# Optimization experiments

Measured on AMD Instinct MI355X. Metric: run time of the kernel, lower is better.

The kernel has to match this reference:

```python
import jax, jax.numpy as jnp
import numpy as np

D_MODEL = 1024
N_HEADS = 16
D_K = D_MODEL // N_HEADS
LOCAL_WINDOW = 128
GLOBAL_TOKENS = 16


def sparse_mask(seq_len):
    i = jnp.arange(seq_len)[:, None]
    j = jnp.arange(seq_len)[None, :]
    local = jnp.abs(i - j) <= LOCAL_WINDOW
    glob = (i < GLOBAL_TOKENS) | (j < GLOBAL_TOKENS)
    causal = j <= i
    return ((local | glob) & causal)[None, None]  # [1,1,S,S]


def setup_inputs() -> dict:
    key = jax.random.key(0)
    ks = jax.random.split(key, 11)
    B, S = 2, 2048
    std = 1.0 / np.sqrt(D_MODEL)
    inp = {
        'query': jax.random.normal(ks[0], (B, S, D_MODEL), jnp.float32),
        'key': jax.random.normal(ks[1], (B, S, D_MODEL), jnp.float32),
        'value': jax.random.normal(ks[2], (B, S, D_MODEL), jnp.float32),
        'w_q': jax.random.normal(ks[3], (D_MODEL, D_MODEL), jnp.float32) * std,
        'b_q': jnp.zeros((D_MODEL,), jnp.float32),
        'w_k': jax.random.normal(ks[4], (D_MODEL, D_MODEL), jnp.float32) * std,
        'b_k': jnp.zeros((D_MODEL,), jnp.float32),
        'w_v': jax.random.normal(ks[5], (D_MODEL, D_MODEL), jnp.float32) * std,
        'b_v': jnp.zeros((D_MODEL,), jnp.float32),
        'w_o': jax.random.normal(ks[6], (D_MODEL, D_MODEL), jnp.float32) * std,
        'b_o': jnp.zeros((D_MODEL,), jnp.float32),
    }
    return inp


def reference(query, key, value, w_q, b_q, w_k, b_k, w_v, b_v, w_o, b_o):
    B, S, _ = query.shape
    # project and split heads -> [B,H,S,d_k]
    def proj(x, w, b):
        y = x @ w.T + b
        return y.reshape(B, S, N_HEADS, D_K).transpose(0, 2, 1, 3)
    q = proj(query, w_q, b_q)
    k = proj(key, w_k, b_k)
    v = proj(value, w_v, b_v)
    scores = jnp.einsum('bhqd,bhkd->bhqk', q, k) / np.sqrt(D_K).astype(np.float32)
    mask = sparse_mask(S)
    scores = jnp.where(mask, scores, -jnp.inf)
    attn = jax.nn.softmax(scores, axis=-1)
    out = jnp.einsum('bhqk,bhkd->bhqd', attn, v)
    out = out.transpose(0, 2, 1, 3).reshape(B, S, D_MODEL)
    return out @ w_o.T + b_o
```

## Files before the change

kernel.cpp:

```cpp
#include <hip/hip_runtime.h>

typedef unsigned short u16;
typedef u16 u16x8 __attribute__((ext_vector_type(8)));
typedef __bf16 bf16x8 __attribute__((ext_vector_type(8)));
typedef float f32x4 __attribute__((ext_vector_type(4)));

#define MFMA16 __builtin_amdgcn_mfma_f32_16x16x32_bf16

__device__ __forceinline__ u16 f2bf(float f) {
  unsigned u = __builtin_bit_cast(unsigned, f);
  u += 0x7FFFu + ((u >> 16) & 1u);
  return (u16)(u >> 16);
}

__device__ __forceinline__ int swz(int row, int bcol) {
  return row * 128 + (bcol ^ ((row & 7) << 4));
}

__device__ __forceinline__ void gl16(const u16* g, u16* l) {
  __builtin_amdgcn_global_load_lds(
      (const __attribute__((address_space(1))) unsigned int*)g,
      (__attribute__((address_space(3))) unsigned int*)l, 16, 0, 0);
}

__device__ __forceinline__ void BARR() {
  asm volatile("" ::: "memory");
  __builtin_amdgcn_s_barrier();
  asm volatile("" ::: "memory");
}

__global__ __launch_bounds__(256)
void cast7(const float* __restrict__ a0, const float* __restrict__ a1,
           const float* __restrict__ a2, const float* __restrict__ a3,
           const float* __restrict__ a4, const float* __restrict__ a5,
           const float* __restrict__ a6, u16* __restrict__ ws) {
  const int y = blockIdx.y;
  const float* s;
  u16* d;
  int n;
  switch (y) {
    case 0: s = a0; d = ws + 4194304; n = 4194304; break;
    case 1: s = a1; d = ws + 8388608; n = 4194304; break;
    case 2: s = a2; d = ws + 12582912; n = 4194304; break;
    case 3: s = a3; d = ws + 0; n = 1048576; break;
    case 4: s = a4; d = ws + 1048576; n = 1048576; break;
    case 5: s = a5; d = ws + 2097152; n = 1048576; break;
    default: s = a6; d = ws + 3145728; n = 1048576; break;
  }
  const int i = (blockIdx.x * 256 + threadIdx.x) * 8;
  if (i >= n) return;
  float4 v0 = *(const float4*)(s + i);
  float4 v1 = *(const float4*)(s + i + 4);
  u16x8 p = {f2bf(v0.x), f2bf(v0.y), f2bf(v0.z), f2bf(v0.w),
             f2bf(v1.x), f2bf(v1.y), f2bf(v1.z), f2bf(v1.w)};
  *(u16x8*)(d + i) = p;
}

#define STGA(tt, c)                                                         \
  gl16(A + (m0 + (c)*64 + (w << 3) + (lane >> 3)) * 1024 + (tt)*64 +        \
           (((lane & 7) ^ (lane >> 3)) << 3),                               \
       (u16*)(sb + (((tt)&1) << 16) + (c)*8192 + (w << 10)))
#define STGB(tt, c)                                                         \
  gl16(B + (n0 + (c)*64 + (w << 3) + (lane >> 3)) * 1024 + (tt)*64 +        \
           (((lane & 7) ^ (lane >> 3)) << 3),                               \
       (u16*)(sb + (((tt)&1) << 16) + 32768 + (c)*8192 + (w << 10)))

__global__ __launch_bounds__(512)
void qkv_gemm256(const u16* __restrict__ ws_in, const float* __restrict__ c0,
                 const float* __restrict__ c1, const float* __restrict__ c2,
                 u16* __restrict__ o0, u16* __restrict__ o1,
                 u16* __restrict__ o2) {
  const int bid = blockIdx.x;
  const int s = (bid & 7) * 24 + (bid >> 3);
  const int z = s >> 6;
  const int rem = s & 63;
  const int m0 = (rem >> 2) << 8;
  const int n0 = (rem & 3) << 8;

  const u16* __restrict__ A = ws_in + 4194304 + z * 4194304;
  const u16* __restrict__ B = ws_in + z * 1048576;
  const float* Bi = (z == 0) ? c0 : (z == 1) ? c1 : c2;
  u16* O = (z == 0) ? o0 : (z == 1) ? o1 : o2;

  const int tid = threadIdx.x, lane = tid & 63, w = tid >> 6;
  const int wm = w >> 2, wn = w & 3;
  const int r = lane & 15, g = lane >> 4;

  __shared__ u16 SH[65536];
  char* sb = (char*)SH;

  f32x4 acc[8][4] = {};
  bf16x8 af[2][4], bf[2][4];

  const int colr0 = (g * 16) ^ ((r & 7) << 4);
  const int colr1 = (64 + g * 16) ^ ((r & 7) << 4);
  const int rowAb = (wm * 128 + r) * 128;
  const int rowBb = 32768 + (wn * 64 + r) * 128;

#define LDA(half)                                                           \
  _Pragma("unroll") for (int m = 0; m < 4; ++m) {                           \
    char* p = sb + bo + rowAb + ((half)*64 + m * 16) * 128;                 \
    af[0][m] = __builtin_bit_cast(bf16x8, *(const u16x8*)(p + colr0));      \
    af[1][m] = __builtin_bit_cast(bf16x8, *(const u16x8*)(p + colr1));      \
  }
#define LDB(n)                                                              \
  {                                                                         \
    char* p = sb + bo + rowBb + (n)*16 * 128;                               \
    bf[0][n] = __builtin_bit_cast(bf16x8, *(const u16x8*)(p + colr0));      \
    bf[1][n] = __builtin_bit_cast(bf16x8, *(const u16x8*)(p + colr1));      \
  }
#define FMA(mh, nl)                                                         \
  __builtin_amdgcn_s_setprio(1);                                           \
  _Pragma("unroll") for (int m = 0; m < 4; ++m)                             \
  _Pragma("unroll") for (int n = 0; n < 2; ++n) {                           \
    acc[(mh)*4 + m][(nl)*2 + n] =                                           \
        MFMA16(af[0][m], bf[0][(nl)*2 + n], acc[(mh)*4 + m][(nl)*2 + n], 0, \
               0, 0);                                                       \
    acc[(mh)*4 + m][(nl)*2 + n] =                                           \
        MFMA16(af[1][m], bf[1][(nl)*2 + n], acc[(mh)*4 + m][(nl)*2 + n], 0, \
               0, 0);                                                       \
  }                                                                         \
  __builtin_amdgcn_s_setprio(0);

#pragma unroll
  for (int c = 0; c < 4; ++c) STGB(0, c);
#pragma unroll
  for (int c = 0; c < 4; ++c) STGA(0, c);
#pragma unroll
  for (int c = 0; c < 4; ++c) STGB(1, c);
#pragma unroll
  for (int c = 0; c < 4; ++c) STGA(1, c);
  asm volatile("s_waitcnt vmcnt(8)" ::: "memory");
  __builtin_amdgcn_s_barrier();
  asm volatile("" ::: "memory");

  for (int t = 0; t < 16; ++t) {
    const int bo = (t & 1) << 16;
    if (t >= 1 && t < 15) { STGB(t + 1, 0); STGB(t + 1, 1); STGB(t + 1, 2); }
    LDA(0);
    LDB(0);
    LDB(1);
    FMA(0, 0);
    BARR();
    if (t >= 1 && t < 15) { STGB(t + 1, 3); STGA(t + 1, 1); STGA(t + 1, 2); }
    LDB(2);
    LDB(3);
    FMA(0, 1);
    BARR();
    if (t < 14) STGA(t + 2, 0);
    LDA(1);
    FMA(1, 0);
    BARR();
    if (t < 14) STGA(t + 2, 3);
    FMA(1, 1);
    if (t < 14)
      asm volatile("s_waitcnt vmcnt(2)" ::: "memory");
    else
      asm volatile("s_waitcnt vmcnt(0)" ::: "memory");
    BARR();
  }

#pragma unroll
  for (int n = 0; n < 4; ++n) {
    const int gn = n0 + wn * 64 + n * 16 + r;
    const int hh = gn >> 6, d = gn & 63;
    const float bv = Bi[gn];
#pragma unroll
    for (int m = 0; m < 8; ++m) {
#pragma unroll
      for (int q = 0; q < 4; ++q) {
        int gm = m0 + wm * 128 + m * 16 + g * 4 + q;
        int bb = gm >> 11, sIdx = gm & 2047;
        O[((bb * 16 + hh) * 2048 + sIdx) * 64 + d] = f2bf(acc[m][n][q] + bv);
      }
    }
  }
#undef LDA
#undef LDB
#undef FMA
}

struct GemmAcc {
  f32x4 acc[4][4];
};

__device__ __forceinline__ void gemm_core(const u16* __restrict__ A,
                                          const u16* __restrict__ B, int m0,
                                          int n0, u16* As, u16* Bs,
                                          GemmAcc& R) {
  const int tid = threadIdx.x, lane = tid & 63, w = tid >> 6;
  const int wr = w >> 1, wc = w & 1;
  const int r = lane & 15, g = lane >> 4;
  const int crow = lane >> 3;
  const int ce = ((lane & 7) ^ crow) * 8;
  const u16* Ag = A + (m0 + w * 32 + crow) * 1024 + ce;
  const u16* Bg = B + (n0 + w * 32 + crow) * 1024 + ce;
  u16* Al = As + w * 2048;
  u16* Bl = Bs + w * 2048;

  for (int kt = 0; kt < 16; ++kt) {
    __syncthreads();
#pragma unroll
    for (int i = 0; i < 4; ++i) {
      gl16(Ag + kt * 64 + i * 8192, Al + i * 512);
      gl16(Bg + kt * 64 + i * 8192, Bl + i * 512);
    }
    __syncthreads();
#pragma unroll
    for (int kk = 0; kk < 2; ++kk) {
      bf16x8 af[4], bfr[4];
#pragma unroll
      for (int m = 0; m < 4; ++m)
        af[m] = __builtin_bit_cast(
            bf16x8, *(const u16x8*)((char*)As +
                                    swz(wr * 64 + m * 16 + r, kk * 64 + g * 16)));
#pragma unroll
      for (int n = 0; n < 4; ++n)
        bfr[n] = __builtin_bit_cast(
            bf16x8, *(const u16x8*)((char*)Bs +
                                    swz(wc * 64 + n * 16 + r, kk * 64 + g * 16)));
#pragma unroll
      for (int m = 0; m < 4; ++m)
#pragma unroll
        for (int n = 0; n < 4; ++n)
          R.acc[m][n] = MFMA16(af[m], bfr[n], R.acc[m][n], 0, 0, 0);
    }
  }
}

__global__ __launch_bounds__(256)
void out_gemm(const u16* __restrict__ A, const u16* __restrict__ W,
              const float* __restrict__ Bi, float* __restrict__ C) {
  const int m0 = blockIdx.y * 128, n0 = blockIdx.x * 128;
  const int tid = threadIdx.x, lane = tid & 63, w = tid >> 6;
  const int wr = w >> 1, wc = w & 1;
  const int r = lane & 15, g = lane >> 4;

  __shared__ u16 As[128 * 64];
  __shared__ u16 Bs[128 * 64];

  GemmAcc R = {};
  gemm_core(A, W, m0, n0, As, Bs, R);

#pragma unroll
  for (int m = 0; m < 4; ++m) {
#pragma unroll
    for (int n = 0; n < 4; ++n) {
      int gn = n0 + wc * 64 + n * 16 + r;
      float bv = Bi[gn];
#pragma unroll
      for (int q = 0; q < 4; ++q) {
        int gm = m0 + wr * 64 + m * 16 + g * 4 + q;
        C[gm * 1024 + gn] = R.acc[m][n][q] + bv;
      }
    }
  }
}

__global__ __launch_bounds__(256)
void attn_kernel(const u16* __restrict__ Q, const u16* __restrict__ K,
                 const u16* __restrict__ V, u16* __restrict__ O) {
  const int qt = blockIdx.x, h = blockIdx.y, b = blockIdx.z;
  const int tid = threadIdx.x, lane = tid & 63, w = tid >> 6;
  const int r = lane & 15, g = lane >> 4;
  const int q0 = qt * 64;
  const int base = (b * 16 + h) * 131072;
  const u16* Qb = Q + base;
  const u16* Kb = K + base;
  const u16* Vb = V + base;

  __shared__ u16 Ks[64 * 64];
  __shared__ u16 Vt[64 * 64];
  __shared__ u16 Pl[4608];

  bf16x8 qf[2];
  {
    const u16* qp = Qb + (q0 + w * 16 + r) * 64 + g * 8;
    qf[0] = __builtin_bit_cast(bf16x8, *(const u16x8*)qp);
    qf[1] = __builtin_bit_cast(bf16x8, *(const u16x8*)(qp + 32));
  }

  f32x4 acc[4] = {};
  float m_run[4] = {-1e30f, -1e30f, -1e30f, -1e30f};
  float l_run[4] = {};

  const int nt = (qt <= 3) ? (qt + 1) : 4;
  const int srow = tid >> 3, sc = (tid & 7) * 8;

  for (int tix = 0; tix < nt; ++tix) {
    const int t = (tix == 0) ? 0 : ((qt <= 3) ? tix : (qt - 3 + tix));
    const int j0 = t * 64;
    __syncthreads();
#pragma unroll
    for (int i = 0; i < 2; ++i) {
      int row = i * 32 + srow;
      u16x8 kv = *(const u16x8*)(Kb + (j0 + row) * 64 + sc);
      *(u16x8*)((char*)Ks + swz(row, sc * 2)) = kv;
      u16x8 vv = *(const u16x8*)(Vb + (j0 + row) * 64 + sc);
#pragma unroll
      for (int qq = 0; qq < 8; ++qq) {
        int d = sc + qq;
        *(u16*)((char*)Vt + d * 128 + ((2 * row) ^ ((d & 7) << 4))) = vv[qq];
      }
    }
    __syncthreads();

    f32x4 S[4] = {};
#pragma unroll
    for (int kk = 0; kk < 2; ++kk)
#pragma unroll
      for (int n = 0; n < 4; ++n) {
        bf16x8 kf = __builtin_bit_cast(
            bf16x8,
            *(const u16x8*)((char*)Ks + swz(n * 16 + r, kk * 64 + g * 16)));
        S[n] = MFMA16(qf[kk], kf, S[n], 0, 0, 0);
      }

    float mloc[4] = {-1e30f, -1e30f, -1e30f, -1e30f};
#pragma unroll
    for (int n = 0; n < 4; ++n) {
      int j = j0 + n * 16 + r;
#pragma unroll
      for (int q = 0; q < 4; ++q) {
        int i = q0 + w * 16 + g * 4 + q;
        bool ok = (j <= i) && (((i - j) <= 128) || (j < 16));
        float s = ok ? S[n][q] * 0.125f : -1e30f;
        S[n][q] = s;
        mloc[q] = fmaxf(mloc[q], s);
      }
    }
#pragma unroll
    for (int q = 0; q < 4; ++q)
#pragma unroll
      for (int off = 1; off < 16; off <<= 1)
        mloc[q] = fmaxf(mloc[q], __shfl_xor(mloc[q], off));

    float alpha[4], rsum[4] = {};
#pragma unroll
    for (int q = 0; q < 4; ++q) {
      float mn = fmaxf(m_run[q], mloc[q]);
      alpha[q] = __expf(m_run[q] - mn);
      m_run[q] = mn;
    }
#pragma unroll
    for (int n = 0; n < 4; ++n)
#pragma unroll
      for (int q = 0; q < 4; ++q) {
        float p = __expf(S[n][q] - m_run[q]);
        S[n][q] = p;
        rsum[q] += p;
      }
#pragma unroll
    for (int q = 0; q < 4; ++q) {
#pragma unroll
      for (int off = 1; off < 16; off <<= 1)
        rsum[q] += __shfl_xor(rsum[q], off);
      l_run[q] = l_run[q] * alpha[q] + rsum[q];
    }
#pragma unroll
    for (int n = 0; n < 4; ++n) {
      acc[n][0] *= alpha[0];
      acc[n][1] *= alpha[1];
      acc[n][2] *= alpha[2];
      acc[n][3] *= alpha[3];
    }

#pragma unroll
    for (int n = 0; n < 4; ++n)
#pragma unroll
      for (int q = 0; q < 4; ++q)
        *((u16*)((char*)Pl + w * 2304 + (g * 4 + q) * 144) + (n * 16 + r)) =
            f2bf(S[n][q]);

#pragma unroll
    for (int kk = 0; kk < 2; ++kk) {
      bf16x8 pf = __builtin_bit_cast(
          bf16x8,
          *(const u16x8*)((char*)Pl + w * 2304 + r * 144 + kk * 64 + g * 16));
#pragma unroll
      for (int n = 0; n < 4; ++n) {
        bf16x8 vf = __builtin_bit_cast(
            bf16x8,
            *(const u16x8*)((char*)Vt + swz(n * 16 + r, kk * 64 + g * 16)));
        acc[n] = MFMA16(pf, vf, acc[n], 0, 0, 0);
      }
    }
  }

#pragma unroll
  for (int n = 0; n < 4; ++n)
#pragma unroll
    for (int q = 0; q < 4; ++q) {
      int s = q0 + w * 16 + g * 4 + q;
      int d = n * 16 + r;
      O[(b * 2048 + s) * 1024 + h * 64 + d] = f2bf(acc[n][q] / l_run[q]);
    }
}

extern "C" void kernel_launch(void* const* d_in, const int* in_sizes, int n_in,
                              void* d_out, int out_size, void* d_ws,
                              size_t ws_size, hipStream_t stream) {
  const float* b_q = (const float*)d_in[4];
  const float* b_k = (const float*)d_in[6];
  const float* b_v = (const float*)d_in[8];
  const float* b_o = (const float*)d_in[10];

  u16* ws = (u16*)d_ws;
  u16* Qw = ws + 16777216;
  u16* Kw = ws + 20971520;
  u16* Vw = ws + 25165824;
  u16* Aw = ws + 4194304;

  cast7<<<dim3(2048, 7), dim3(256), 0, stream>>>(
      (const float*)d_in[0], (const float*)d_in[1], (const float*)d_in[2],
      (const float*)d_in[3], (const float*)d_in[5], (const float*)d_in[7],
      (const float*)d_in[9], ws);
  qkv_gemm256<<<dim3(192), dim3(512), 0, stream>>>(ws, b_q, b_k, b_v, Qw, Kw,
                                                   Vw);
  attn_kernel<<<dim3(32, 16, 2), dim3(256), 0, stream>>>(Qw, Kw, Vw, Aw);
  out_gemm<<<dim3(8, 32), dim3(256), 0, stream>>>(Aw, ws + 3145728, b_o,
                                                  (float*)d_out);
}
```

Measured before the change: 105.1 us.

## Pipeline output GEMM with double-buffered async loads and restructure QKV GEMM schedule

Replaces the output projection GEMM, which synchronized around every k-tile load, with a double-buffered pipeline that issues direct global-to-LDS loads for upcoming tiles while MFMAs run on the current buffer. It also remaps block indices so neighbouring blocks share tiles in cache. Separately, the QKV GEMM loop drops from four barrier phases to two, with shallower prefetch (one tile ahead instead of two). This is meant to hide global-load latency in the output GEMM and cut barrier overhead in the QKV GEMM. The risk is that the shallower QKV prefetch exposes more memory latency.

```diff
diff --git a/kernel.cpp b/kernel.cpp
--- a/kernel.cpp
+++ b/kernel.cpp
@@ -28,6 +28,7 @@
   __builtin_amdgcn_s_barrier();
   asm volatile("" ::: "memory");
 }
+#define VMCNT(n) asm volatile("s_waitcnt vmcnt(" #n ")" ::: "memory")
 
 __global__ __launch_bounds__(256)
 void cast7(const float* __restrict__ a0, const float* __restrict__ a1,
@@ -109,16 +110,14 @@
     bf[0][n] = __builtin_bit_cast(bf16x8, *(const u16x8*)(p + colr0));      \
     bf[1][n] = __builtin_bit_cast(bf16x8, *(const u16x8*)(p + colr1));      \
   }
-#define FMA(mh, nl)                                                         \
-  __builtin_amdgcn_s_setprio(1);                                           \
+#define FMAH(h)                                                             \
+  __builtin_amdgcn_s_setprio(1);                                            \
   _Pragma("unroll") for (int m = 0; m < 4; ++m)                             \
-  _Pragma("unroll") for (int n = 0; n < 2; ++n) {                           \
-    acc[(mh)*4 + m][(nl)*2 + n] =                                           \
-        MFMA16(af[0][m], bf[0][(nl)*2 + n], acc[(mh)*4 + m][(nl)*2 + n], 0, \
-               0, 0);                                                       \
-    acc[(mh)*4 + m][(nl)*2 + n] =                                           \
-        MFMA16(af[1][m], bf[1][(nl)*2 + n], acc[(mh)*4 + m][(nl)*2 + n], 0, \
-               0, 0);                                                       \
+  _Pragma("unroll") for (int n = 0; n < 4; ++n) {                           \
+    acc[(h)*4 + m][n] = MFMA16(af[0][m], bf[0][n], acc[(h)*4 + m][n], 0, 0, \
+                               0);                                          \
+    acc[(h)*4 + m][n] = MFMA16(af[1][m], bf[1][n], acc[(h)*4 + m][n], 0, 0, \
+                               0);                                          \
   }                                                                         \
   __builtin_amdgcn_s_setprio(0);
 
@@ -126,37 +125,22 @@
   for (int c = 0; c < 4; ++c) STGB(0, c);
 #pragma unroll
   for (int c = 0; c < 4; ++c) STGA(0, c);
-#pragma unroll
-  for (int c = 0; c < 4; ++c) STGB(1, c);
-#pragma unroll
-  for (int c = 0; c < 4; ++c) STGA(1, c);
-  asm volatile("s_waitcnt vmcnt(8)" ::: "memory");
+  VMCNT(0);
   __builtin_amdgcn_s_barrier();
   asm volatile("" ::: "memory");
 
   for (int t = 0; t < 16; ++t) {
     const int bo = (t & 1) << 16;
-    if (t >= 1 && t < 15) { STGB(t + 1, 0); STGB(t + 1, 1); STGB(t + 1, 2); }
+    if (t < 15) { STGB(t + 1, 0); STGB(t + 1, 1); STGB(t + 1, 2); STGB(t + 1, 3); }
     LDA(0);
-    LDB(0);
-    LDB(1);
-    FMA(0, 0);
+    LDB(0); LDB(1); LDB(2); LDB(3);
+    FMAH(0);
+    if (t < 15) { VMCNT(4); } else { VMCNT(0); }
     BARR();
-    if (t >= 1 && t < 15) { STGB(t + 1, 3); STGA(t + 1, 1); STGA(t + 1, 2); }
-    LDB(2);
-    LDB(3);
-    FMA(0, 1);
-    BARR();
-    if (t < 14) STGA(t + 2, 0);
+    if (t < 15) { STGA(t + 1, 0); STGA(t + 1, 2); STGA(t + 1, 1); STGA(t + 1, 3); }
     LDA(1);
-    FMA(1, 0);
-    BARR();
-    if (t < 14) STGA(t + 2, 3);
-    FMA(1, 1);
-    if (t < 14)
-      asm volatile("s_waitcnt vmcnt(2)" ::: "memory");
-    else
-      asm volatile("s_waitcnt vmcnt(0)" ::: "memory");
+    FMAH(1);
+    if (t < 15) { VMCNT(2); }
     BARR();
   }
 
@@ -177,84 +161,104 @@
   }
 #undef LDA
 #undef LDB
-#undef FMA
-}
-
-struct GemmAcc {
-  f32x4 acc[4][4];
-};
-
-__device__ __forceinline__ void gemm_core(const u16* __restrict__ A,
-                                          const u16* __restrict__ B, int m0,
-                                          int n0, u16* As, u16* Bs,
-                                          GemmAcc& R) {
+#undef FMAH
+}
+
+#define OSTGA(tt, c, j)                                                     \
+  gl16(Ain + (m0 + (c)*64 + (w << 4) + (j)*8 + (lane >> 3)) * 1024 +        \
+           (tt)*64 + (((lane & 7) ^ (lane >> 3)) << 3),                     \
+       (u16*)(sb + (((tt)&1) << 15) + (c)*8192 + (w << 11) + ((j) << 10)))
+#define OSTGB(tt, c, j)                                                     \
+  gl16(W + (n0 + (c)*64 + (w << 4) + (j)*8 + (lane >> 3)) * 1024 +          \
+           (tt)*64 + (((lane & 7) ^ (lane >> 3)) << 3),                     \
+       (u16*)(sb + (((tt)&1) << 15) + 16384 + (c)*8192 + (w << 11) +        \
+              ((j) << 10)))
+
+__global__ __launch_bounds__(256)
+void out_gemm_p(const u16* __restrict__ Ain, const u16* __restrict__ W,
+                const float* __restrict__ Bi, float* __restrict__ C) {
+  const int bid = blockIdx.x;
+  const int s = (bid & 7) * 32 + (bid >> 3);
+  const int m0 = (s >> 3) << 7, n0 = (s & 7) << 7;
+
   const int tid = threadIdx.x, lane = tid & 63, w = tid >> 6;
-  const int wr = w >> 1, wc = w & 1;
+  const int wm = w >> 1, wn = w & 1;
   const int r = lane & 15, g = lane >> 4;
-  const int crow = lane >> 3;
-  const int ce = ((lane & 7) ^ crow) * 8;
-  const u16* Ag = A + (m0 + w * 32 + crow) * 1024 + ce;
-  const u16* Bg = B + (n0 + w * 32 + crow) * 1024 + ce;
-  u16* Al = As + w * 2048;
-  u16* Bl = Bs + w * 2048;
-
-  for (int kt = 0; kt < 16; ++kt) {
-    __syncthreads();
-#pragma unroll
-    for (int i = 0; i < 4; ++i) {
-      gl16(Ag + kt * 64 + i * 8192, Al + i * 512);
-      gl16(Bg + kt * 64 + i * 8192, Bl + i * 512);
-    }
-    __syncthreads();
-#pragma unroll
-    for (int kk = 0; kk < 2; ++kk) {
-      bf16x8 af[4], bfr[4];
-#pragma unroll
-      for (int m = 0; m < 4; ++m)
-        af[m] = __builtin_bit_cast(
-            bf16x8, *(const u16x8*)((char*)As +
-                                    swz(wr * 64 + m * 16 + r, kk * 64 + g * 16)));
-#pragma unroll
-      for (int n = 0; n < 4; ++n)
-        bfr[n] = __builtin_bit_cast(
-            bf16x8, *(const u16x8*)((char*)Bs +
-                                    swz(wc * 64 + n * 16 + r, kk * 64 + g * 16)));
-#pragma unroll
-      for (int m = 0; m < 4; ++m)
-#pragma unroll
-        for (int n = 0; n < 4; ++n)
-          R.acc[m][n] = MFMA16(af[m], bfr[n], R.acc[m][n], 0, 0, 0);
-    }
-  }
-}
-
-__global__ __launch_bounds__(256)
-void out_gemm(const u16* __restrict__ A, const u16* __restrict__ W,
-              const float* __restrict__ Bi, float* __restrict__ C) {
-  const int m0 = blockIdx.y * 128, n0 = blockIdx.x * 128;
-  const int tid = threadIdx.x, lane = tid & 63, w = tid >> 6;
-  const int wr = w >> 1, wc = w & 1;
-  const int r = lane & 15, g = lane >> 4;
-
-  __shared__ u16 As[128 * 64];
-  __shared__ u16 Bs[128 * 64];
-
-  GemmAcc R = {};
-  gemm_core(A, W, m0, n0, As, Bs, R);
+
+  __shared__ u16 SH[32768];
+  char* sb = (char*)SH;
+
+  f32x4 acc[4][4] = {};
+  bf16x8 af[2][4], bf[2][4];
+
+  const int colr0 = (g * 16) ^ ((r & 7) << 4);
+  const int colr1 = (64 + g * 16) ^ ((r & 7) << 4);
+  const int rowAb = (wm * 64 + r) * 128;
+  const int rowBb = 16384 + (wn * 64 + r) * 128;
+
+#define OLDA()                                                              \
+  _Pragma("unroll") for (int m = 0; m < 4; ++m) {                           \
+    char* p = sb + bo + rowAb + m * 16 * 128;                               \
+    af[0][m] = __builtin_bit_cast(bf16x8, *(const u16x8*)(p + colr0));      \
+    af[1][m] = __builtin_bit_cast(bf16x8, *(const u16x8*)(p + colr1));      \
+  }
+#define OLDB(n)                                                             \
+  {                                                                         \
+    char* p = sb + bo + rowBb + (n)*16 * 128;                               \
+    bf[0][n] = __builtin_bit_cast(bf16x8, *(const u16x8*)(p + colr0));      \
+    bf[1][n] = __builtin_bit_cast(bf16x8, *(const u16x8*)(p + colr1));      \
+  }
+#define OFMA(nh)                                                            \
+  __builtin_amdgcn_s_setprio(1);                                            \
+  _Pragma("unroll") for (int m = 0; m < 4; ++m)                             \
+  _Pragma("unroll") for (int n = 0; n < 2; ++n) {                           \
+    acc[m][(nh)*2 + n] =                                                    \
+        MFMA16(af[0][m], bf[0][(nh)*2 + n], acc[m][(nh)*2 + n], 0, 0, 0);   \
+    acc[m][(nh)*2 + n] =                                                    \
+        MFMA16(af[1][m], bf[1][(nh)*2 + n], acc[m][(nh)*2 + n], 0, 0, 0);   \
+  }                                                                         \
+  __builtin_amdgcn_s_setprio(0);
+
+#pragma unroll
+  for (int c = 0; c < 2; ++c) { OSTGA(0, c, 0); OSTGA(0, c, 1); }
+#pragma unroll
+  for (int c = 0; c < 2; ++c) { OSTGB(0, c, 0); OSTGB(0, c, 1); }
+#pragma unroll
+  for (int c = 0; c < 2; ++c) { OSTGA(1, c, 0); OSTGA(1, c, 1); }
+  VMCNT(4);
+  __builtin_amdgcn_s_barrier();
+  asm volatile("" ::: "memory");
+
+  for (int t = 0; t < 16; ++t) {
+    const int bo = (t & 1) << 15;
+    if (t < 15) { OSTGB(t + 1, 0, 0); OSTGB(t + 1, 0, 1); OSTGB(t + 1, 1, 0); OSTGB(t + 1, 1, 1); }
+    OLDA();
+    OLDB(0); OLDB(1);
+    OFMA(0);
+    BARR();
+    if (t < 14) { OSTGA(t + 2, 0, 0); OSTGA(t + 2, 0, 1); OSTGA(t + 2, 1, 0); OSTGA(t + 2, 1, 1); }
+    OLDB(2); OLDB(3);
+    OFMA(1);
+    if (t < 14) { VMCNT(4); } else if (t == 14) { VMCNT(0); }
+    BARR();
+  }
 
 #pragma unroll
   for (int m = 0; m < 4; ++m) {
 #pragma unroll
     for (int n = 0; n < 4; ++n) {
-      int gn = n0 + wc * 64 + n * 16 + r;
+      int gn = n0 + wn * 64 + n * 16 + r;
       float bv = Bi[gn];
 #pragma unroll
       for (int q = 0; q < 4; ++q) {
-        int gm = m0 + wr * 64 + m * 16 + g * 4 + q;
-        C[gm * 1024 + gn] = R.acc[m][n][q] + bv;
-      }
-    }
-  }
+        int gm = m0 + wm * 64 + m * 16 + g * 4 + q;
+        C[gm * 1024 + gn] = acc[m][n][q] + bv;
+      }
+    }
+  }
+#undef OLDA
+#undef OLDB
+#undef OFMA
 }
 
 __global__ __launch_bounds__(256)
@@ -418,6 +422,6 @@
   qkv_gemm256<<<dim3(192), dim3(512), 0, stream>>>(ws, b_q, b_k, b_v, Qw, Kw,
                                                    Vw);
   attn_kernel<<<dim3(32, 16, 2), dim3(256), 0, stream>>>(Qw, Kw, Vw, Aw);
-  out_gemm<<<dim3(8, 32), dim3(256), 0, stream>>>(Aw, ws + 3145728, b_o,
+  out_gemm_p<<<dim3(256), dim3(256), 0, stream>>>(Aw, ws + 3145728, b_o,
                                                   (float*)d_out);
 }
```

Result: faster. 96.04 us (-8.6%).
